# Performance work log

Measured on AMD Instinct MI355X. Metric: run time of the kernel, lower is better.

The kernel has to match this reference:

```python
import jax, jax.numpy as jnp
import numpy as np
import math

# Static config (matches init_kwargs / input_specs)
SPATIAL = [(64, 64), (32, 32), (16, 16), (8, 8)]  # (H_l, W_l)
BN, LQ, C, M, L, P = 2, 4000, 256, 8, 4, 4
D = C // M  # 32, dim per head


def _bilinear_sample(vflat, H, W, loc):
    """grid_sample(mode=bilinear, padding=zeros, align_corners=False).
    vflat: [N, H*W, M, D]; loc: [N, Lq, M, P, 2] normalized in [0,1].
    Returns [N, Lq, M, P, D].
    Note: grid = 2*loc-1, then x = (g+1)*W/2 - 0.5 == loc*W - 0.5."""
    x = loc[..., 0] * W - 0.5
    y = loc[..., 1] * H - 0.5
    x0f = jnp.floor(x)
    y0f = jnp.floor(y)
    tx = x - x0f
    ty = y - y0f
    x0 = x0f.astype(jnp.int32)
    y0 = y0f.astype(jnp.int32)
    nidx = jnp.arange(vflat.shape[0])[:, None, None, None]
    midx = jnp.arange(vflat.shape[2])[None, None, :, None]
    out = jnp.zeros(loc.shape[:-1] + (vflat.shape[-1],), vflat.dtype)
    for dx, dy, w in ((0, 0, (1 - tx) * (1 - ty)), (1, 0, tx * (1 - ty)),
                      (0, 1, (1 - tx) * ty), (1, 1, tx * ty)):
        xi = x0 + dx
        yi = y0 + dy
        valid = (xi >= 0) & (xi < W) & (yi >= 0) & (yi < H)
        xc = jnp.clip(xi, 0, W - 1)
        yc = jnp.clip(yi, 0, H - 1)
        g = vflat[nidx, yc * W + xc, midx]  # [N,Lq,M,P,D]
        out = out + (w * valid)[..., None] * g
    return out


def setup_inputs() -> dict:
    key = jax.random.key(0)
    ks = jax.random.split(key, 16)
    Lin = sum(h * w for h, w in SPATIAL)
    s = 0.02
    inp = {
        'query': jax.random.normal(ks[0], (BN, LQ, C), jnp.float32),
        'reference_points': jax.random.uniform(ks[1], (BN, LQ, L, 2), jnp.float32),
        'input_flatten': jax.random.normal(ks[2], (BN, Lin, C), jnp.float32),
        'input_spatial_shapes': jnp.array(SPATIAL, jnp.int32),
        'input_level_start_index': jnp.array(
            np.cumsum([0] + [h * w for h, w in SPATIAL[:-1]]), jnp.int32),
        'Wv': jax.random.normal(ks[3], (C, C), jnp.float32) * s,
        'bv': jnp.zeros((C,), jnp.float32),
        'Wk': jax.random.normal(ks[4], (C, C), jnp.float32) * s,
        'bk': jnp.zeros((C,), jnp.float32),
        'Wq': jax.random.normal(ks[5], (C, C), jnp.float32) * s,
        'bq': jnp.zeros((C,), jnp.float32),
        'Woff': jax.random.normal(ks[6], (C, M * L * P * 2), jnp.float32) * s,
        'boff': jax.random.normal(ks[7], (M * L * P * 2,), jnp.float32) * 0.5,
        'Wout': jax.random.normal(ks[8], (C, C), jnp.float32) * s,
        'bout': jnp.zeros((C,), jnp.float32),
    }
    return inp


def _forward(query, reference_points, input_flatten,
             Wv, bv, Wk, bk, Wq, bq, Woff, boff, Wout, bout):
    N, Lq, _ = query.shape
    Lin = input_flatten.shape[1]
    value = (input_flatten @ Wv + bv).reshape(N, Lin, M, D)
    keyf = (input_flatten @ Wk + bk).reshape(N, Lin, M, D)
    q = (query @ Wq + bq).reshape(N, Lq, M, D)
    # sampling locations: ref + offsets / [W_l, H_l]
    off = (query @ Woff + boff).reshape(N, Lq, M, L, P, 2)
    norm = jnp.array([[w, h] for h, w in SPATIAL], jnp.float32)  # [L,2]
    loc = reference_points[:, :, None, :, None, :] + off / norm[None, None, None, :, None, :]
    sk_list, sv_list = [], []
    start = 0
    for lid, (H, W) in enumerate(SPATIAL):
        vl = value[:, start:start + H * W]   # [N,HW,M,D]
        kl = keyf[:, start:start + H * W]
        loc_l = loc[:, :, :, lid]            # [N,Lq,M,P,2]
        sv_list.append(_bilinear_sample(vl, H, W, loc_l))
        sk_list.append(_bilinear_sample(kl, H, W, loc_l))
        start += H * W
    sk = jnp.stack(sk_list, axis=3)  # [N,Lq,M,L,P,D]
    sv = jnp.stack(sv_list, axis=3)
    # key-aware attention: per-query softmax over the L*P sampled keys
    logits = jnp.einsum('nqmd,nqmlpd->nqmlp', q, sk) / math.sqrt(D)
    attn = jax.nn.softmax(logits.reshape(N, Lq, M, L * P), axis=-1)
    out = jnp.einsum('nqmk,nqmkd->nqmd', attn, sv.reshape(N, Lq, M, L * P, D))
    out = out.reshape(N, Lq, C) @ Wout + bout
    return out


def reference(query, reference_points, input_flatten, input_spatial_shapes,
              input_level_start_index, Wv, bv, Wk, bk, Wq, bq, Woff, boff,
              Wout, bout):
    return _forward(query, reference_points, input_flatten,
                    Wv, bv, Wk, bk, Wq, bq, Woff, boff, Wout, bout)
```

## Files before the change

kernel.cpp:

```cpp
#include <hip/hip_runtime.h>

#define NB   2
#define LQN  4000
#define CC   256
#define LIN  5440
#define ROWS1 (NB * LIN)
#define ROWS2 (NB * LQN)
#define ELEMS1 (ROWS1 * CC)

typedef short bf16x8 __attribute__((ext_vector_type(8)));
typedef float f32x4 __attribute__((ext_vector_type(4)));
typedef float f32x2 __attribute__((ext_vector_type(2)));
typedef unsigned short u16x8 __attribute__((ext_vector_type(8)));

__device__ __forceinline__ unsigned short f2b(float f) {
    union { float f; unsigned u; } v; v.f = f;
    unsigned r = v.u + 0x7FFFu + ((v.u >> 16) & 1u);
    return (unsigned short)(r >> 16);
}
__device__ __forceinline__ float b2f(unsigned short u) {
    union { unsigned u; float f; } v; v.u = ((unsigned)u) << 16; return v.f;
}
__device__ __forceinline__ f32x2 b2f2(unsigned int p) {
    union { unsigned u; float f; } lo, hi;
    lo.u = p << 16;
    hi.u = p & 0xFFFF0000u;
    return (f32x2){lo.f, hi.f};
}

__global__ __launch_bounds__(256) void prep(
    const float* __restrict__ xflat, const float* __restrict__ query,
    const float* __restrict__ Wv, const float* __restrict__ Wk,
    const float* __restrict__ Wq, const float* __restrict__ Wo,
    const float* __restrict__ Wout,
    unsigned short* __restrict__ Ab, unsigned short* __restrict__ WT)
{
    const int bx = blockIdx.x, tid = threadIdx.x;
    if (bx < 2360) {
        const size_t e = (size_t)bx * 2048 + (size_t)tid * 8;
        const float* src = (e < ELEMS1) ? xflat + e : query + (e - ELEMS1);
        float4 a = *(const float4*)src;
        float4 b = *(const float4*)(src + 4);
        bf16x8 o;
        o[0] = (short)f2b(a.x); o[1] = (short)f2b(a.y);
        o[2] = (short)f2b(a.z); o[3] = (short)f2b(a.w);
        o[4] = (short)f2b(b.x); o[5] = (short)f2b(b.y);
        o[6] = (short)f2b(b.z); o[7] = (short)f2b(b.w);
        *(bf16x8*)&Ab[e] = o;
    } else {
        const int b2 = bx - 2360;
        const int mat = b2 >> 4;
        const int tile = b2 & 15;
        const int r0 = (tile >> 2) * 64;
        const int c0 = (tile & 3) * 64;
        const float* W = (mat == 0) ? Wv : (mat == 1) ? Wk : (mat == 2) ? Wq
                       : (mat == 3) ? Wo : Wout;
        __shared__ unsigned short t[64][66];
        const int cl = tid & 63, rw = tid >> 6;
        #pragma unroll
        for (int i = 0; i < 16; ++i) {
            const int row = rw * 16 + i;
            t[row][cl] = f2b(W[(size_t)(r0 + row) * 256 + c0 + cl]);
        }
        __syncthreads();
        #pragma unroll
        for (int i = 0; i < 16; ++i) {
            const int n = rw * 16 + i;
            WT[mat * 65536 + (c0 + n) * 256 + r0 + cl] = t[cl][n];
        }
    }
}

__global__ __launch_bounds__(256) void gemm_pw(
    const unsigned short* __restrict__ Ab,
    const unsigned short* __restrict__ WT,
    const float* __restrict__ bv, const float* __restrict__ bk,
    const float* __restrict__ bq, const float* __restrict__ bo,
    unsigned short* __restrict__ value, unsigned short* __restrict__ keyf,
    float* __restrict__ qproj, float* __restrict__ offp)
{
    const int bx = blockIdx.x;
    const int tid = threadIdx.x;
    const int w = tid >> 6, lane = tid & 63;
    const int m16 = lane & 15, q4 = lane >> 4;

    int mat, rowTile, rowBase;
    if (bx < 340) { mat = bx & 1; rowTile = bx >> 1; rowBase = rowTile * 64; }
    else { const int b2 = bx - 340; mat = 2 + (b2 & 1); rowTile = b2 >> 1; rowBase = ROWS1 + rowTile * 64; }

    const unsigned short* Ap = Ab + (size_t)(rowBase + m16) * 256 + q4 * 8;
    const unsigned short* Bp = WT + (size_t)mat * 65536 + (size_t)(w * 64 + m16) * 256 + q4 * 8;

    f32x4 acc[4][4];
    #pragma unroll
    for (int i = 0; i < 4; ++i)
        #pragma unroll
        for (int j = 0; j < 4; ++j) acc[i][j] = (f32x4){0.f, 0.f, 0.f, 0.f};

    bf16x8 aC[4], bC[4], aN[4], bN[4];
    #pragma unroll
    for (int rt = 0; rt < 4; ++rt) aC[rt] = *(const bf16x8*)(Ap + rt * (16 * 256));
    #pragma unroll
    for (int ct = 0; ct < 4; ++ct) bC[ct] = *(const bf16x8*)(Bp + ct * (16 * 256));

    #pragma unroll
    for (int kt = 0; kt < 8; ++kt) {
        if (kt < 7) {
            const int k1 = (kt + 1) * 32;
            #pragma unroll
            for (int rt = 0; rt < 4; ++rt) aN[rt] = *(const bf16x8*)(Ap + rt * (16 * 256) + k1);
            #pragma unroll
            for (int ct = 0; ct < 4; ++ct) bN[ct] = *(const bf16x8*)(Bp + ct * (16 * 256) + k1);
        }
        #pragma unroll
        for (int rt = 0; rt < 4; ++rt)
            #pragma unroll
            for (int ct = 0; ct < 4; ++ct)
                acc[rt][ct] = __builtin_amdgcn_mfma_f32_16x16x32_bf16(aC[rt], bC[ct], acc[rt][ct], 0, 0, 0);
        if (kt < 7) {
            #pragma unroll
            for (int rt = 0; rt < 4; ++rt) aC[rt] = aN[rt];
            #pragma unroll
            for (int ct = 0; ct < 4; ++ct) bC[ct] = bN[ct];
        }
    }

    const int row0l = rowTile * 64;
    if (mat <= 1) {
        unsigned short* C = mat ? keyf : value;
        const float* bias = mat ? bk : bv;
        #pragma unroll
        for (int ct = 0; ct < 4; ++ct) {
            const int col = w * 64 + ct * 16 + m16;
            const float bcol = bias[col];
            #pragma unroll
            for (int rt = 0; rt < 4; ++rt)
                #pragma unroll
                for (int e = 0; e < 4; ++e) {
                    const int r = row0l + rt * 16 + q4 * 4 + e;
                    C[(size_t)r * 256 + col] = f2b(acc[rt][ct][e] + bcol);
                }
        }
    } else {
        float* C = (mat == 3) ? offp : qproj;
        const float* bias = (mat == 3) ? bo : bq;
        #pragma unroll
        for (int ct = 0; ct < 4; ++ct) {
            const int col = w * 64 + ct * 16 + m16;
            const float bcol = bias[col];
            #pragma unroll
            for (int rt = 0; rt < 4; ++rt)
                #pragma unroll
                for (int e = 0; e < 4; ++e) {
                    const int r = row0l + rt * 16 + q4 * 4 + e;
                    C[(size_t)r * 256 + col] = acc[rt][ct][e] + bcol;
                }
        }
    }
}

__global__ __launch_bounds__(512) void gemm_outm(
    const unsigned short* __restrict__ Am,
    const unsigned short* __restrict__ WoT,
    const float* __restrict__ bias, float* __restrict__ C)
{
    const int bx = blockIdx.x;
    const int tid = threadIdx.x;
    const int w = tid >> 6, lane = tid & 63;
    const int m16 = lane & 15, q4 = lane >> 4;
    const int col0 = w * 32;

    const unsigned short* Ap = Am + (size_t)bx * (16 * 256) + m16 * 256 + q4 * 8;
    const unsigned short* Bp = WoT + (size_t)(col0 + m16) * 256 + q4 * 8;

    f32x4 acc[2];
    acc[0] = (f32x4){0.f, 0.f, 0.f, 0.f};
    acc[1] = (f32x4){0.f, 0.f, 0.f, 0.f};

    bf16x8 aC, bC[2], aN, bN[2];
    aC = *(const bf16x8*)Ap;
    bC[0] = *(const bf16x8*)Bp;
    bC[1] = *(const bf16x8*)(Bp + 16 * 256);

    #pragma unroll
    for (int kt = 0; kt < 8; ++kt) {
        if (kt < 7) {
            const int k1 = (kt + 1) * 32;
            aN = *(const bf16x8*)(Ap + k1);
            bN[0] = *(const bf16x8*)(Bp + k1);
            bN[1] = *(const bf16x8*)(Bp + 16 * 256 + k1);
        }
        acc[0] = __builtin_amdgcn_mfma_f32_16x16x32_bf16(aC, bC[0], acc[0], 0, 0, 0);
        acc[1] = __builtin_amdgcn_mfma_f32_16x16x32_bf16(aC, bC[1], acc[1], 0, 0, 0);
        if (kt < 7) { aC = aN; bC[0] = bN[0]; bC[1] = bN[1]; }
    }

    #pragma unroll
    for (int ct = 0; ct < 2; ++ct) {
        const int col = col0 + ct * 16 + m16;
        const float bcol = bias[col];
        #pragma unroll
        for (int e = 0; e < 4; ++e) {
            const int r = bx * 16 + q4 * 4 + e;
            C[(size_t)r * 256 + col] = acc[ct][e] + bcol;
        }
    }
}

__global__ __launch_bounds__(256) void sample_attn(
    const float* __restrict__ qproj,
    const float* __restrict__ offp,
    const float* __restrict__ refp,
    const unsigned short* __restrict__ value,
    const unsigned short* __restrict__ keyf,
    unsigned short* __restrict__ outmid)
{
    const int bx = blockIdx.x;
    const int tid = threadIdx.x;
    const int q0 = bx * 2;

    __shared__ float s_off[2][256];
    __shared__ float s_ref[2][8];
    __shared__ __align__(16) float s_w[2][8][16][4];
    __shared__ __align__(16) int   s_idx[2][8][16][4];

    s_off[0][tid] = offp[(size_t)q0 * 256 + tid];
    s_off[1][tid] = offp[(size_t)(q0 + 1) * 256 + tid];
    if (tid < 16) s_ref[tid >> 3][tid & 7] = refp[q0 * 8 + tid];
    __syncthreads();

    {
        const int qi = tid >> 7, wt = tid & 127;
        const int pm = wt >> 4, l = (wt >> 2) & 3, p = wt & 3;
        const int HW = 64 >> l;
        const int st = (l == 0) ? 0 : (l == 1) ? 4096 : (l == 2) ? 5120 : 5376;
        const float fHW = (float)HW;
        float x = s_ref[qi][l * 2 + 0] * fHW + s_off[qi][pm * 32 + l * 8 + p * 2 + 0] - 0.5f;
        float y = s_ref[qi][l * 2 + 1] * fHW + s_off[qi][pm * 32 + l * 8 + p * 2 + 1] - 0.5f;
        float x0f = floorf(x), y0f = floorf(y);
        float txf = x - x0f, tyf = y - y0f;
        int x0 = (int)x0f, y0 = (int)y0f;
        int x1 = x0 + 1, y1 = y0 + 1;
        float fx0 = (x0 >= 0 && x0 < HW) ? (1.f - txf) : 0.f;
        float fx1 = (x1 >= 0 && x1 < HW) ? txf : 0.f;
        float fy0 = (y0 >= 0 && y0 < HW) ? (1.f - tyf) : 0.f;
        float fy1 = (y1 >= 0 && y1 < HW) ? tyf : 0.f;
        int xc0 = min(max(x0, 0), HW - 1), xc1 = min(max(x1, 0), HW - 1);
        int yc0 = min(max(y0, 0), HW - 1), yc1 = min(max(y1, 0), HW - 1);
        const int pt = l * 4 + p;
        s_w[qi][pm][pt][0] = fx0 * fy0;
        s_w[qi][pm][pt][1] = fx1 * fy0;
        s_w[qi][pm][pt][2] = fx0 * fy1;
        s_w[qi][pm][pt][3] = fx1 * fy1;
        const int eb = pm * 32;
        s_idx[qi][pm][pt][0] = (st + yc0 * HW + xc0) * CC + eb;
        s_idx[qi][pm][pt][1] = (st + yc0 * HW + xc1) * CC + eb;
        s_idx[qi][pm][pt][2] = (st + yc1 * HW + xc0) * CC + eb;
        s_idx[qi][pm][pt][3] = (st + yc1 * HW + xc1) * CC + eb;
    }
    __syncthreads();

    const int qi = tid >> 7, t = tid & 127;
    const int m = t >> 4, p2 = (t >> 2) & 3, dq = t & 3;
    const int qrow = q0 + qi;
    const int n = bx / (LQN / 2);
    const size_t nbase = (size_t)n * LIN * CC;
    const unsigned short* vbp = value + nbase;
    const unsigned short* kbp = keyf + nbase;
    const int doff = dq * 8;

    const float* qp = &qproj[(size_t)qrow * 256 + m * 32 + doff];
    const float4 qa = *(const float4*)qp;
    const float4 qb = *(const float4*)(qp + 4);
    const f32x2 q01 = (f32x2){qa.x, qa.y};
    const f32x2 q23 = (f32x2){qa.z, qa.w};
    const f32x2 q45 = (f32x2){qb.x, qb.y};
    const f32x2 q67 = (f32x2){qb.z, qb.w};

    float lg[4];
    f32x2 vv0[4], vv1[4], vv2[4], vv3[4];

    #pragma unroll
    for (int r = 0; r < 4; ++r) {
        const int pt = r * 4 + p2;
        const float4 w4 = *(const float4*)&s_w[qi][m][pt][0];
        const int4  i4 = *(const int4*)&s_idx[qi][m][pt][0];
        const f32x2 w0 = (f32x2){w4.x, w4.x};
        const f32x2 w1 = (f32x2){w4.y, w4.y};
        const f32x2 w2 = (f32x2){w4.z, w4.z};
        const f32x2 w3 = (f32x2){w4.w, w4.w};
        const uint4 ka = *(const uint4*)(kbp + i4.x + doff);
        const uint4 kb = *(const uint4*)(kbp + i4.y + doff);
        const uint4 kc = *(const uint4*)(kbp + i4.z + doff);
        const uint4 kd = *(const uint4*)(kbp + i4.w + doff);
        const uint4 va = *(const uint4*)(vbp + i4.x + doff);
        const uint4 vb = *(const uint4*)(vbp + i4.y + doff);
        const uint4 vc = *(const uint4*)(vbp + i4.z + doff);
        const uint4 vd = *(const uint4*)(vbp + i4.w + doff);
        f32x2 ks0 = __builtin_elementwise_fma(w3, b2f2(kd.x),
                    __builtin_elementwise_fma(w2, b2f2(kc.x),
                    __builtin_elementwise_fma(w1, b2f2(kb.x), w0 * b2f2(ka.x))));
        f32x2 ks1 = __builtin_elementwise_fma(w3, b2f2(kd.y),
                    __builtin_elementwise_fma(w2, b2f2(kc.y),
                    __builtin_elementwise_fma(w1, b2f2(kb.y), w0 * b2f2(ka.y))));
        f32x2 ks2 = __builtin_elementwise_fma(w3, b2f2(kd.z),
                    __builtin_elementwise_fma(w2, b2f2(kc.z),
                    __builtin_elementwise_fma(w1, b2f2(kb.z), w0 * b2f2(ka.z))));
        f32x2 ks3 = __builtin_elementwise_fma(w3, b2f2(kd.w),
                    __builtin_elementwise_fma(w2, b2f2(kc.w),
                    __builtin_elementwise_fma(w1, b2f2(kb.w), w0 * b2f2(ka.w))));
        vv0[r]    = __builtin_elementwise_fma(w3, b2f2(vd.x),
                    __builtin_elementwise_fma(w2, b2f2(vc.x),
                    __builtin_elementwise_fma(w1, b2f2(vb.x), w0 * b2f2(va.x))));
        vv1[r]    = __builtin_elementwise_fma(w3, b2f2(vd.y),
                    __builtin_elementwise_fma(w2, b2f2(vc.y),
                    __builtin_elementwise_fma(w1, b2f2(vb.y), w0 * b2f2(va.y))));
        vv2[r]    = __builtin_elementwise_fma(w3, b2f2(vd.z),
                    __builtin_elementwise_fma(w2, b2f2(vc.z),
                    __builtin_elementwise_fma(w1, b2f2(vb.z), w0 * b2f2(va.z))));
        vv3[r]    = __builtin_elementwise_fma(w3, b2f2(vd.w),
                    __builtin_elementwise_fma(w2, b2f2(vc.w),
                    __builtin_elementwise_fma(w1, b2f2(vb.w), w0 * b2f2(va.w))));
        f32x2 d2 = __builtin_elementwise_fma(q67, ks3,
                   __builtin_elementwise_fma(q45, ks2,
                   __builtin_elementwise_fma(q23, ks1, q01 * ks0)));
        float s = d2.x + d2.y;
        s += __shfl_xor(s, 1);
        s += __shfl_xor(s, 2);
        lg[r] = s * 0.17677669529663687f;
    }

    float mx = fmaxf(fmaxf(lg[0], lg[1]), fmaxf(lg[2], lg[3]));
    mx = fmaxf(mx, __shfl_xor(mx, 4));
    mx = fmaxf(mx, __shfl_xor(mx, 8));
    float e0 = __expf(lg[0] - mx), e1 = __expf(lg[1] - mx);
    float e2 = __expf(lg[2] - mx), e3 = __expf(lg[3] - mx);
    float Z = e0 + e1 + e2 + e3;
    Z += __shfl_xor(Z, 4);
    Z += __shfl_xor(Z, 8);

    const f32x2 ee0 = (f32x2){e0, e0}, ee1 = (f32x2){e1, e1};
    const f32x2 ee2 = (f32x2){e2, e2}, ee3 = (f32x2){e3, e3};
    f32x2 o0 = __builtin_elementwise_fma(ee3, vv0[3],
               __builtin_elementwise_fma(ee2, vv0[2],
               __builtin_elementwise_fma(ee1, vv0[1], ee0 * vv0[0])));
    f32x2 o1 = __builtin_elementwise_fma(ee3, vv1[3],
               __builtin_elementwise_fma(ee2, vv1[2],
               __builtin_elementwise_fma(ee1, vv1[1], ee0 * vv1[0])));
    f32x2 o2 = __builtin_elementwise_fma(ee3, vv2[3],
               __builtin_elementwise_fma(ee2, vv2[2],
               __builtin_elementwise_fma(ee1, vv2[1], ee0 * vv2[0])));
    f32x2 o3 = __builtin_elementwise_fma(ee3, vv3[3],
               __builtin_elementwise_fma(ee2, vv3[2],
               __builtin_elementwise_fma(ee1, vv3[1], ee0 * vv3[0])));

    float a0 = o0.x, a1 = o0.y, a2 = o1.x, a3 = o1.y;
    float a4 = o2.x, a5 = o2.y, a6 = o3.x, a7 = o3.y;
    #pragma unroll
    for (int msk = 4; msk <= 8; msk <<= 1) {
        a0 += __shfl_xor(a0, msk);
        a1 += __shfl_xor(a1, msk);
        a2 += __shfl_xor(a2, msk);
        a3 += __shfl_xor(a3, msk);
        a4 += __shfl_xor(a4, msk);
        a5 += __shfl_xor(a5, msk);
        a6 += __shfl_xor(a6, msk);
        a7 += __shfl_xor(a7, msk);
    }
    if (p2 == 0) {
        const float rz = 1.0f / Z;
        u16x8 res;
        res[0] = f2b(a0 * rz); res[1] = f2b(a1 * rz);
        res[2] = f2b(a2 * rz); res[3] = f2b(a3 * rz);
        res[4] = f2b(a4 * rz); res[5] = f2b(a5 * rz);
        res[6] = f2b(a6 * rz); res[7] = f2b(a7 * rz);
        *(u16x8*)&outmid[(size_t)qrow * 256 + m * 32 + doff] = res;
    }
}

extern "C" void kernel_launch(void* const* d_in, const int* in_sizes, int n_in,
                              void* d_out, int out_size, void* d_ws, size_t ws_size,
                              hipStream_t stream) {
    const float* query = (const float*)d_in[0];
    const float* refp  = (const float*)d_in[1];
    const float* xflat = (const float*)d_in[2];
    const float* Wv   = (const float*)d_in[5];
    const float* bv   = (const float*)d_in[6];
    const float* Wk   = (const float*)d_in[7];
    const float* bk   = (const float*)d_in[8];
    const float* Wq   = (const float*)d_in[9];
    const float* bq   = (const float*)d_in[10];
    const float* Woff = (const float*)d_in[11];
    const float* boff = (const float*)d_in[12];
    const float* Wout = (const float*)d_in[13];
    const float* bout = (const float*)d_in[14];

    char* ws = (char*)d_ws;
    unsigned short* value  = (unsigned short*)ws; ws += (size_t)ROWS1 * CC * 2;
    unsigned short* keyf   = (unsigned short*)ws; ws += (size_t)ROWS1 * CC * 2;
    float* qproj  = (float*)ws; ws += (size_t)ROWS2 * CC * 4;
    float* offp   = (float*)ws; ws += (size_t)ROWS2 * CC * 4;
    unsigned short* outmid = (unsigned short*)ws; ws += (size_t)ROWS2 * CC * 2;
    unsigned short* Ab = (unsigned short*)ws; ws += (size_t)(ROWS1 + ROWS2) * CC * 2;
    unsigned short* WT = (unsigned short*)ws; ws += 5 * 65536 * 2;

    dim3 blk(256);

    prep<<<dim3(2360 + 80), blk, 0, stream>>>(xflat, query, Wv, Wk, Wq, Woff, Wout, Ab, WT);

    gemm_pw<<<dim3(340 + 250), blk, 0, stream>>>(
        Ab, WT, bv, bk, bq, boff, value, keyf, qproj, offp);

    sample_attn<<<dim3(NB * LQN / 2), blk, 0, stream>>>(qproj, offp, refp, value, keyf, outmid);

    gemm_outm<<<dim3(ROWS2 / 16), dim3(512), 0, stream>>>(
        outmid, WT + 4 * 65536, bout, (float*)d_out);
}
```

Measured before the change: 160.7 us.

## Interleave key and value per head into one buffer, one query per block

The key and value projections are written into one interleaved kv buffer. Each head's 32 key channels sit next to its 32 value channels in a 512-wide row, so one gather fetches both key and value for a sampled corner. sample_attn now handles one query per block and splits key and value lanes across 8 threads per point. Lane shuffles then exchange the softmax weights so the value lanes can do the weighted sum. This trades the separate key and value gathers for single wider contiguous loads, at the cost of extra shuffles and twice as many blocks, each doing half the per-block setup.

Result: no change. 163.8 us (+2.0%).

```diff
diff --git a/kernel.cpp b/kernel.cpp
--- a/kernel.cpp
+++ b/kernel.cpp
@@ -76,7 +76,7 @@
     const unsigned short* __restrict__ WT,
     const float* __restrict__ bv, const float* __restrict__ bk,
     const float* __restrict__ bq, const float* __restrict__ bo,
-    unsigned short* __restrict__ value, unsigned short* __restrict__ keyf,
+    unsigned short* __restrict__ kv,
     float* __restrict__ qproj, float* __restrict__ offp)
 {
     const int bx = blockIdx.x;
@@ -127,18 +127,19 @@
 
     const int row0l = rowTile * 64;
     if (mat <= 1) {
-        unsigned short* C = mat ? keyf : value;
         const float* bias = mat ? bk : bv;
+        const int vhalf = (mat == 0) ? 32 : 0;
         #pragma unroll
         for (int ct = 0; ct < 4; ++ct) {
             const int col = w * 64 + ct * 16 + m16;
             const float bcol = bias[col];
+            const int cb = (col >> 5) * 64 + vhalf + (col & 31);
             #pragma unroll
             for (int rt = 0; rt < 4; ++rt)
                 #pragma unroll
                 for (int e = 0; e < 4; ++e) {
                     const int r = row0l + rt * 16 + q4 * 4 + e;
-                    C[(size_t)r * 256 + col] = f2b(acc[rt][ct][e] + bcol);
+                    kv[(size_t)r * 512 + cb] = f2b(acc[rt][ct][e] + bcol);
                 }
         }
     } else {
@@ -211,32 +212,29 @@
     const float* __restrict__ qproj,
     const float* __restrict__ offp,
     const float* __restrict__ refp,
-    const unsigned short* __restrict__ value,
-    const unsigned short* __restrict__ keyf,
+    const unsigned short* __restrict__ kv,
     unsigned short* __restrict__ outmid)
 {
     const int bx = blockIdx.x;
     const int tid = threadIdx.x;
-    const int q0 = bx * 2;
-
-    __shared__ float s_off[2][256];
-    __shared__ float s_ref[2][8];
-    __shared__ __align__(16) float s_w[2][8][16][4];
-    __shared__ __align__(16) int   s_idx[2][8][16][4];
-
-    s_off[0][tid] = offp[(size_t)q0 * 256 + tid];
-    s_off[1][tid] = offp[(size_t)(q0 + 1) * 256 + tid];
-    if (tid < 16) s_ref[tid >> 3][tid & 7] = refp[q0 * 8 + tid];
+
+    __shared__ float s_off[256];
+    __shared__ float s_ref[8];
+    __shared__ __align__(16) float s_w[8][16][4];
+    __shared__ __align__(16) int   s_idx[8][16][4];
+
+    const int baseq = bx * CC;
+    s_off[tid] = offp[baseq + tid];
+    if (tid < 8) s_ref[tid] = refp[bx * 8 + tid];
     __syncthreads();
 
-    {
-        const int qi = tid >> 7, wt = tid & 127;
-        const int pm = wt >> 4, l = (wt >> 2) & 3, p = wt & 3;
+    if (tid < 128) {
+        const int pm = tid >> 4, l = (tid >> 2) & 3, p = tid & 3;
         const int HW = 64 >> l;
         const int st = (l == 0) ? 0 : (l == 1) ? 4096 : (l == 2) ? 5120 : 5376;
         const float fHW = (float)HW;
-        float x = s_ref[qi][l * 2 + 0] * fHW + s_off[qi][pm * 32 + l * 8 + p * 2 + 0] - 0.5f;
-        float y = s_ref[qi][l * 2 + 1] * fHW + s_off[qi][pm * 32 + l * 8 + p * 2 + 1] - 0.5f;
+        float x = s_ref[l * 2 + 0] * fHW + s_off[pm * 32 + l * 8 + p * 2 + 0] - 0.5f;
+        float y = s_ref[l * 2 + 1] * fHW + s_off[pm * 32 + l * 8 + p * 2 + 1] - 0.5f;
         float x0f = floorf(x), y0f = floorf(y);
         float txf = x - x0f, tyf = y - y0f;
         int x0 = (int)x0f, y0 = (int)y0f;
@@ -248,28 +246,25 @@
         int xc0 = min(max(x0, 0), HW - 1), xc1 = min(max(x1, 0), HW - 1);
         int yc0 = min(max(y0, 0), HW - 1), yc1 = min(max(y1, 0), HW - 1);
         const int pt = l * 4 + p;
-        s_w[qi][pm][pt][0] = fx0 * fy0;
-        s_w[qi][pm][pt][1] = fx1 * fy0;
-        s_w[qi][pm][pt][2] = fx0 * fy1;
-        s_w[qi][pm][pt][3] = fx1 * fy1;
-        const int eb = pm * 32;
-        s_idx[qi][pm][pt][0] = (st + yc0 * HW + xc0) * CC + eb;
-        s_idx[qi][pm][pt][1] = (st + yc0 * HW + xc1) * CC + eb;
-        s_idx[qi][pm][pt][2] = (st + yc1 * HW + xc0) * CC + eb;
-        s_idx[qi][pm][pt][3] = (st + yc1 * HW + xc1) * CC + eb;
+        s_w[pm][pt][0] = fx0 * fy0;
+        s_w[pm][pt][1] = fx1 * fy0;
+        s_w[pm][pt][2] = fx0 * fy1;
+        s_w[pm][pt][3] = fx1 * fy1;
+        const int hb = pm * 64;
+        s_idx[pm][pt][0] = (st + yc0 * HW + xc0) * 512 + hb;
+        s_idx[pm][pt][1] = (st + yc0 * HW + xc1) * 512 + hb;
+        s_idx[pm][pt][2] = (st + yc1 * HW + xc0) * 512 + hb;
+        s_idx[pm][pt][3] = (st + yc1 * HW + xc1) * 512 + hb;
     }
     __syncthreads();
 
-    const int qi = tid >> 7, t = tid & 127;
-    const int m = t >> 4, p2 = (t >> 2) & 3, dq = t & 3;
-    const int qrow = q0 + qi;
-    const int n = bx / (LQN / 2);
-    const size_t nbase = (size_t)n * LIN * CC;
-    const unsigned short* vbp = value + nbase;
-    const unsigned short* kbp = keyf + nbase;
-    const int doff = dq * 8;
-
-    const float* qp = &qproj[(size_t)qrow * 256 + m * 32 + doff];
+    const int m = tid >> 5, p2 = (tid >> 3) & 3, dq8 = tid & 7;
+    const int n = bx / LQN;
+    const unsigned short* kvb = kv + (size_t)n * LIN * 512;
+    const int doff = dq8 * 8;
+    const int qoff = (dq8 & 3) * 8;
+
+    const float* qp = &qproj[baseq + m * 32 + qoff];
     const float4 qa = *(const float4*)qp;
     const float4 qb = *(const float4*)(qp + 4);
     const f32x2 q01 = (f32x2){qa.x, qa.y};
@@ -283,47 +278,32 @@
     #pragma unroll
     for (int r = 0; r < 4; ++r) {
         const int pt = r * 4 + p2;
-        const float4 w4 = *(const float4*)&s_w[qi][m][pt][0];
-        const int4  i4 = *(const int4*)&s_idx[qi][m][pt][0];
+        const float4 w4 = *(const float4*)&s_w[m][pt][0];
+        const int4  i4 = *(const int4*)&s_idx[m][pt][0];
         const f32x2 w0 = (f32x2){w4.x, w4.x};
         const f32x2 w1 = (f32x2){w4.y, w4.y};
         const f32x2 w2 = (f32x2){w4.z, w4.z};
         const f32x2 w3 = (f32x2){w4.w, w4.w};
-        const uint4 ka = *(const uint4*)(kbp + i4.x + doff);
-        const uint4 kb = *(const uint4*)(kbp + i4.y + doff);
-        const uint4 kc = *(const uint4*)(kbp + i4.z + doff);
-        const uint4 kd = *(const uint4*)(kbp + i4.w + doff);
-        const uint4 va = *(const uint4*)(vbp + i4.x + doff);
-        const uint4 vb = *(const uint4*)(vbp + i4.y + doff);
-        const uint4 vc = *(const uint4*)(vbp + i4.z + doff);
-        const uint4 vd = *(const uint4*)(vbp + i4.w + doff);
-        f32x2 ks0 = __builtin_elementwise_fma(w3, b2f2(kd.x),
-                    __builtin_elementwise_fma(w2, b2f2(kc.x),
-                    __builtin_elementwise_fma(w1, b2f2(kb.x), w0 * b2f2(ka.x))));
-        f32x2 ks1 = __builtin_elementwise_fma(w3, b2f2(kd.y),
-                    __builtin_elementwise_fma(w2, b2f2(kc.y),
-                    __builtin_elementwise_fma(w1, b2f2(kb.y), w0 * b2f2(ka.y))));
-        f32x2 ks2 = __builtin_elementwise_fma(w3, b2f2(kd.z),
-                    __builtin_elementwise_fma(w2, b2f2(kc.z),
-                    __builtin_elementwise_fma(w1, b2f2(kb.z), w0 * b2f2(ka.z))));
-        f32x2 ks3 = __builtin_elementwise_fma(w3, b2f2(kd.w),
-                    __builtin_elementwise_fma(w2, b2f2(kc.w),
-                    __builtin_elementwise_fma(w1, b2f2(kb.w), w0 * b2f2(ka.w))));
-        vv0[r]    = __builtin_elementwise_fma(w3, b2f2(vd.x),
-                    __builtin_elementwise_fma(w2, b2f2(vc.x),
-                    __builtin_elementwise_fma(w1, b2f2(vb.x), w0 * b2f2(va.x))));
-        vv1[r]    = __builtin_elementwise_fma(w3, b2f2(vd.y),
-                    __builtin_elementwise_fma(w2, b2f2(vc.y),
-                    __builtin_elementwise_fma(w1, b2f2(vb.y), w0 * b2f2(va.y))));
-        vv2[r]    = __builtin_elementwise_fma(w3, b2f2(vd.z),
-                    __builtin_elementwise_fma(w2, b2f2(vc.z),
-                    __builtin_elementwise_fma(w1, b2f2(vb.z), w0 * b2f2(va.z))));
-        vv3[r]    = __builtin_elementwise_fma(w3, b2f2(vd.w),
-                    __builtin_elementwise_fma(w2, b2f2(vc.w),
-                    __builtin_elementwise_fma(w1, b2f2(vb.w), w0 * b2f2(va.w))));
-        f32x2 d2 = __builtin_elementwise_fma(q67, ks3,
-                   __builtin_elementwise_fma(q45, ks2,
-                   __builtin_elementwise_fma(q23, ks1, q01 * ks0)));
+        const uint4 A = *(const uint4*)(kvb + i4.x + doff);
+        const uint4 B = *(const uint4*)(kvb + i4.y + doff);
+        const uint4 Cc = *(const uint4*)(kvb + i4.z + doff);
+        const uint4 D = *(const uint4*)(kvb + i4.w + doff);
+        f32x2 c0 = __builtin_elementwise_fma(w3, b2f2(D.x),
+                   __builtin_elementwise_fma(w2, b2f2(Cc.x),
+                   __builtin_elementwise_fma(w1, b2f2(B.x), w0 * b2f2(A.x))));
+        f32x2 c1 = __builtin_elementwise_fma(w3, b2f2(D.y),
+                   __builtin_elementwise_fma(w2, b2f2(Cc.y),
+                   __builtin_elementwise_fma(w1, b2f2(B.y), w0 * b2f2(A.y))));
+        f32x2 c2 = __builtin_elementwise_fma(w3, b2f2(D.z),
+                   __builtin_elementwise_fma(w2, b2f2(Cc.z),
+                   __builtin_elementwise_fma(w1, b2f2(B.z), w0 * b2f2(A.z))));
+        f32x2 c3 = __builtin_elementwise_fma(w3, b2f2(D.w),
+                   __builtin_elementwise_fma(w2, b2f2(Cc.w),
+                   __builtin_elementwise_fma(w1, b2f2(B.w), w0 * b2f2(A.w))));
+        vv0[r] = c0; vv1[r] = c1; vv2[r] = c2; vv3[r] = c3;
+        f32x2 d2 = __builtin_elementwise_fma(q67, c3,
+                   __builtin_elementwise_fma(q45, c2,
+                   __builtin_elementwise_fma(q23, c1, q01 * c0)));
         float s = d2.x + d2.y;
         s += __shfl_xor(s, 1);
         s += __shfl_xor(s, 2);
@@ -331,16 +311,20 @@
     }
 
     float mx = fmaxf(fmaxf(lg[0], lg[1]), fmaxf(lg[2], lg[3]));
-    mx = fmaxf(mx, __shfl_xor(mx, 4));
     mx = fmaxf(mx, __shfl_xor(mx, 8));
+    mx = fmaxf(mx, __shfl_xor(mx, 16));
     float e0 = __expf(lg[0] - mx), e1 = __expf(lg[1] - mx);
     float e2 = __expf(lg[2] - mx), e3 = __expf(lg[3] - mx);
     float Z = e0 + e1 + e2 + e3;
-    Z += __shfl_xor(Z, 4);
     Z += __shfl_xor(Z, 8);
-
-    const f32x2 ee0 = (f32x2){e0, e0}, ee1 = (f32x2){e1, e1};
-    const f32x2 ee2 = (f32x2){e2, e2}, ee3 = (f32x2){e3, e3};
+    Z += __shfl_xor(Z, 16);
+
+    const float E0 = __shfl_xor(e0, 4), E1 = __shfl_xor(e1, 4);
+    const float E2 = __shfl_xor(e2, 4), E3 = __shfl_xor(e3, 4);
+    const float Zr = __shfl_xor(Z, 4);
+
+    const f32x2 ee0 = (f32x2){E0, E0}, ee1 = (f32x2){E1, E1};
+    const f32x2 ee2 = (f32x2){E2, E2}, ee3 = (f32x2){E3, E3};
     f32x2 o0 = __builtin_elementwise_fma(ee3, vv0[3],
                __builtin_elementwise_fma(ee2, vv0[2],
                __builtin_elementwise_fma(ee1, vv0[1], ee0 * vv0[0])));
@@ -357,7 +341,7 @@
     float a0 = o0.x, a1 = o0.y, a2 = o1.x, a3 = o1.y;
     float a4 = o2.x, a5 = o2.y, a6 = o3.x, a7 = o3.y;
     #pragma unroll
-    for (int msk = 4; msk <= 8; msk <<= 1) {
+    for (int msk = 8; msk <= 16; msk <<= 1) {
         a0 += __shfl_xor(a0, msk);
         a1 += __shfl_xor(a1, msk);
         a2 += __shfl_xor(a2, msk);
@@ -367,14 +351,14 @@
         a6 += __shfl_xor(a6, msk);
         a7 += __shfl_xor(a7, msk);
     }
-    if (p2 == 0) {
-        const float rz = 1.0f / Z;
+    if ((dq8 & 4) && p2 == 0) {
+        const float rz = 1.0f / Zr;
         u16x8 res;
         res[0] = f2b(a0 * rz); res[1] = f2b(a1 * rz);
         res[2] = f2b(a2 * rz); res[3] = f2b(a3 * rz);
         res[4] = f2b(a4 * rz); res[5] = f2b(a5 * rz);
         res[6] = f2b(a6 * rz); res[7] = f2b(a7 * rz);
-        *(u16x8*)&outmid[(size_t)qrow * 256 + m * 32 + doff] = res;
+        *(u16x8*)&outmid[baseq + m * 32 + qoff] = res;
     }
 }
 
@@ -396,8 +380,7 @@
     const float* bout = (const float*)d_in[14];
 
     char* ws = (char*)d_ws;
-    unsigned short* value  = (unsigned short*)ws; ws += (size_t)ROWS1 * CC * 2;
-    unsigned short* keyf   = (unsigned short*)ws; ws += (size_t)ROWS1 * CC * 2;
+    unsigned short* kv = (unsigned short*)ws; ws += (size_t)ROWS1 * 512 * 2;
     float* qproj  = (float*)ws; ws += (size_t)ROWS2 * CC * 4;
     float* offp   = (float*)ws; ws += (size_t)ROWS2 * CC * 4;
     unsigned short* outmid = (unsigned short*)ws; ws += (size_t)ROWS2 * CC * 2;
@@ -409,9 +392,9 @@
     prep<<<dim3(2360 + 80), blk, 0, stream>>>(xflat, query, Wv, Wk, Wq, Woff, Wout, Ab, WT);
 
     gemm_pw<<<dim3(340 + 250), blk, 0, stream>>>(
-        Ab, WT, bv, bk, bq, boff, value, keyf, qproj, offp);
-
-    sample_attn<<<dim3(NB * LQN / 2), blk, 0, stream>>>(qproj, offp, refp, value, keyf, outmid);
+        Ab, WT, bv, bk, bq, boff, kv, qproj, offp);
+
+    sample_attn<<<dim3(NB * LQN), blk, 0, stream>>>(qproj, offp, refp, kv, outmid);
 
     gemm_outm<<<dim3(ROWS2 / 16), dim3(512), 0, stream>>>(
         outmid, WT + 4 * 65536, bout, (float*)d_out);
```
